# Kernel optimization log

Hardware: AMD Instinct MI355X
Metric: run time of the kernel (lower is better)

Reference implementation:

```python
import jax, jax.numpy as jnp
import numpy as np

NUM_HEADS = 10
LN_EPS = 1e-5


def setup_inputs() -> dict:
    key = jax.random.key(0)
    ks = jax.random.split(key, 6)
    N, D = 4096, 640  # in_dim == out_dim required by residual add
    x = jax.random.normal(ks[0], (N, D), dtype=jnp.float32)
    s = 1.0 / np.sqrt(D)
    Wq = jax.random.normal(ks[1], (D, D), dtype=jnp.float32) * s  # torch Linear weight [out,in]
    Wk = jax.random.normal(ks[2], (D, D), dtype=jnp.float32) * s
    Wv = jax.random.normal(ks[3], (D, D), dtype=jnp.float32) * s
    gamma = jnp.ones((D,), dtype=jnp.float32)
    beta = jnp.zeros((D,), dtype=jnp.float32)
    return {"x": x, "Wq": Wq, "Wk": Wk, "Wv": Wv, "gamma": gamma, "beta": beta}


def reference(x, Wq, Wk, Wv, gamma, beta):
    N, D = x.shape
    dk = D // NUM_HEADS
    Q = x @ Wq.T  # [N, D]
    K = x @ Wk.T
    V = x @ Wv.T
    # Faithful to source: raw reshapes (NOT transposes)
    Qh = Q.reshape(NUM_HEADS, N, dk)
    Kh = K.reshape(NUM_HEADS, N, dk).reshape(NUM_HEADS, dk, N)  # torch.reshape, not .mT
    Vh = V.reshape(NUM_HEADS, N, dk)
    # Faithful quirk: scale by sqrt(K.shape[2]) == sqrt(N)
    scale = np.float32(np.sqrt(N))
    wghts = jax.nn.softmax((Qh @ Kh) / scale, axis=-1)  # [H, N, N]
    values = wghts @ Vh  # [H, N, dk]
    values = values.reshape(N, NUM_HEADS * dk)  # raw reshape merge
    values = values + x  # residual
    # LayerNorm(out_dim), biased variance, eps=1e-5
    mean = jnp.mean(values, axis=-1, keepdims=True)
    var = jnp.mean(jnp.square(values - mean), axis=-1, keepdims=True)
    out = (values - mean) * jax.lax.rsqrt(var + LN_EPS) * gamma + beta
    return out
```

## Files before the change

### kernel.cpp

```cpp
#include <hip/hip_runtime.h>
#if __has_include(<hip/hip_fp8.h>)
#include <hip/hip_fp8.h>
#endif


typedef __bf16 bf16x8 __attribute__((ext_vector_type(8)));
typedef __bf16 bf16x4 __attribute__((ext_vector_type(4)));
typedef float  f32x4  __attribute__((ext_vector_type(4)));
typedef unsigned short u16x4 __attribute__((ext_vector_type(4)));
typedef unsigned int   u32x4 __attribute__((ext_vector_type(4)));
typedef long           la64  __attribute__((may_alias));
typedef unsigned int   ua32  __attribute__((may_alias));

#define N_TOK   4096
#define D_MODEL 640
#define DK      64
#define HSLAB   (N_TOK * DK)
#define SQS 0.15014030f

#if __has_builtin(__builtin_amdgcn_exp2f)
#define EXP2(x) __builtin_amdgcn_exp2f(x)
#else
#define EXP2(x) exp2f(x)
#endif

__device__ __forceinline__ void stage16(const void* g, void* lds_uniform) {
    __builtin_amdgcn_global_load_lds(
        (const __attribute__((address_space(1))) unsigned int*)g,
        (__attribute__((address_space(3))) unsigned int*)lds_uniform, 16, 0, 0);
}

__device__ __forceinline__ u16x4 cvt4(f32x4 v) {
    return __builtin_bit_cast(u16x4, __builtin_convertvector(v, bf16x4));
}

__device__ __forceinline__ unsigned int pk_fp8(f32x4 v) {
#if __has_builtin(__builtin_amdgcn_cvt_pk_fp8_f32)
    int r = 0;
    r = __builtin_amdgcn_cvt_pk_fp8_f32(v[0], v[1], r, false);
    r = __builtin_amdgcn_cvt_pk_fp8_f32(v[2], v[3], r, true);
    return (unsigned int)r;
#else
    union { unsigned char b[4]; unsigned int u; } x;
    x.b[0] = __hip_fp8_e4m3(v[0]).__x;
    x.b[1] = __hip_fp8_e4m3(v[1]).__x;
    x.b[2] = __hip_fp8_e4m3(v[2]).__x;
    x.b[3] = __hip_fp8_e4m3(v[3]).__x;
    return x.u;
#endif
}

__global__ __launch_bounds__(256) void cvt_all(const float* __restrict__ x,
                                               const float* __restrict__ w0,
                                               const float* __restrict__ w1,
                                               const float* __restrict__ w2,
                                               unsigned short* __restrict__ xb,
                                               unsigned short* __restrict__ d0,
                                               unsigned short* __restrict__ d1,
                                               unsigned short* __restrict__ d2,
                                               f32x4* __restrict__ ltot4) {
    int i = blockIdx.x * 256 + threadIdx.x;
    if (i >= 962560) { ltot4[i - 962560] = (f32x4){0.f, 0.f, 0.f, 0.f}; return; }
    const float* s; unsigned short* d; int off; float scl = 1.0f;
    if (i < 655360) { s = x; d = xb; off = i; }
    else {
        int j = i - 655360;
        int w = j / 102400; off = j - w * 102400;
        s = (w == 0) ? w0 : (w == 1) ? w1 : w2;
        d = (w == 0) ? d0 : (w == 1) ? d1 : d2;
        if (w < 2) scl = SQS;
    }
    f32x4 v = ((const f32x4*)s)[off];
    v[0] *= scl; v[1] *= scl; v[2] *= scl; v[3] *= scl;
    ((u16x4*)d)[off] = cvt4(v);
}

__global__ __launch_bounds__(256, 2) void gemm_qkv(
    const unsigned short* __restrict__ xb,
    const unsigned short* __restrict__ wq,
    const unsigned short* __restrict__ wk,
    const unsigned short* __restrict__ wv,
    unsigned short* __restrict__ Qo,
    unsigned short* __restrict__ Ko,
    unsigned short* __restrict__ Vo) {
    const int b = blockIdx.x;
    const int g = b & 31;
    const int r = b >> 5;
    const int mode = r / 5;
    const int m0 = g * 128;
    const int n0 = (r % 5) * 128;
    const unsigned short* W = (mode == 0) ? wq : (mode == 1) ? wk : wv;
    unsigned short*       C = (mode == 0) ? Qo : (mode == 1) ? Ko : Vo;

    __shared__ unsigned short As[8192];
    __shared__ unsigned short Bs[8192];

    const int tid  = threadIdx.x;
    const int lane = tid & 63;
    const int wave = tid >> 6;
    const int quad = lane >> 4, l16 = lane & 15;
    const int wm = (wave >> 1) * 64, wn = (wave & 1) * 64;
    const int swz = l16 & 7;

    f32x4 acc[4][4] = {};

    int prow[4], pcol[4], lbase[4];
    for (int j = 0; j < 4; j++) {
        int p = j * 256 + tid;
        prow[j] = p >> 3;
        pcol[j] = ((p & 7) ^ (prow[j] & 7)) * 8;
        lbase[j] = (j * 256 + wave * 64) * 8;
    }

    for (int kt = 0; kt < D_MODEL; kt += 64) {
        __syncthreads();
        for (int j = 0; j < 4; j++) {
            stage16(&xb[(size_t)(m0 + prow[j]) * D_MODEL + kt + pcol[j]], As + lbase[j]);
            stage16(&W [(size_t)(n0 + prow[j]) * D_MODEL + kt + pcol[j]], Bs + lbase[j]);
        }
        __syncthreads();

        for (int s = 0; s < 2; s++) {
            bf16x8 af[4], bfr[4];
            for (int mi = 0; mi < 4; mi++) {
                int row = wm + mi * 16 + l16;
                af[mi] = *(const bf16x8*)&As[row * 64 + (((s << 2) + quad) ^ swz) * 8];
            }
            for (int ni = 0; ni < 4; ni++) {
                int row = wn + ni * 16 + l16;
                bfr[ni] = *(const bf16x8*)&Bs[row * 64 + (((s << 2) + quad) ^ swz) * 8];
            }
            for (int mi = 0; mi < 4; mi++)
                for (int ni = 0; ni < 4; ni++)
                    acc[mi][ni] = __builtin_amdgcn_mfma_f32_16x16x32_bf16(af[mi], bfr[ni], acc[mi][ni], 0, 0, 0);
        }
    }

    for (int mi = 0; mi < 4; mi++)
        for (int ni = 0; ni < 4; ni++) {
            u16x4 cv = cvt4(acc[mi][ni]);
            for (int r2 = 0; r2 < 4; r2++) {
                int row = m0 + wm + mi * 16 + quad * 4 + r2;
                int col = n0 + wn + ni * 16 + l16;
                C[(size_t)row * D_MODEL + col] = cv[r2];
            }
        }
}

__global__ __launch_bounds__(256) void transpose_kv(
    const unsigned short* __restrict__ Kn, unsigned char* __restrict__ Kp8,
    const unsigned short* __restrict__ Vn, unsigned char* __restrict__ Vp8,
    const unsigned short* __restrict__ Qn, unsigned char* __restrict__ Qf8) {
    const int z = blockIdx.z;
    const int t = threadIdx.x;

    if (z >= 20) {
        const size_t base = (size_t)(z - 20) * HSLAB + blockIdx.x * 4096 + t * 16;
        bf16x8 v0 = *(const bf16x8*)&Qn[base];
        bf16x8 v1 = *(const bf16x8*)&Qn[base + 8];
        f32x4 a = {(float)v0[0], (float)v0[1], (float)v0[2], (float)v0[3]};
        f32x4 b = {(float)v0[4], (float)v0[5], (float)v0[6], (float)v0[7]};
        f32x4 c = {(float)v1[0], (float)v1[1], (float)v1[2], (float)v1[3]};
        f32x4 d = {(float)v1[4], (float)v1[5], (float)v1[6], (float)v1[7]};
        u32x4 o = {pk_fp8(a), pk_fp8(b), pk_fp8(c), pk_fp8(d)};
        *(u32x4*)&Qf8[base] = o;
        return;
    }

    __shared__ unsigned short T[64][66];
    const unsigned short* src; unsigned char* dst;
    int R, Cc, r0, c0;
    if (z < 10) { src = Kn; dst = Kp8; R = 64;   Cc = 4096; r0 = 0; c0 = blockIdx.x * 64; }
    else        { src = Vn; dst = Vp8; R = 4096; Cc = 64;   r0 = blockIdx.x * 64; c0 = 0; }
    const size_t hb = (size_t)(z % 10) * HSLAB;
    const int rr = t >> 3, c8 = (t & 7) * 8;

    for (int hf = 0; hf < 2; hf++) {
        int r = rr + hf * 32;
        bf16x8 v = *(const bf16x8*)&src[hb + (size_t)(r0 + r) * Cc + c0 + c8];
        for (int j = 0; j < 8; j++) T[r][c8 + j] = ((unsigned short*)&v)[j];
    }
    __syncthreads();
    const bf16x8 zz = {};
    for (int hf = 0; hf < 2; hf++) {
        int r = rr + hf * 32;
        *(bf16x8*)&((unsigned short*)src)[hb + (size_t)(r0 + r) * Cc + c0 + c8] = zz;
    }
    for (int hf = 0; hf < 2; hf++) {
        int oc = rr + hf * 32;
        f32x4 lo, hi;
        for (int j = 0; j < 4; j++) {
            lo[j] = __builtin_bit_cast(float, (unsigned int)T[c8 + j][oc] << 16);
            hi[j] = __builtin_bit_cast(float, (unsigned int)T[c8 + 4 + j][oc] << 16);
        }
        uint2 ov; ov.x = pk_fp8(lo); ov.y = pk_fp8(hi);
        size_t dcol = (z < 10) ? ((size_t)(c0 + oc) * 64 + r0 + c8)
                               : ((size_t)oc * 4096 + r0 + c8);
        *(uint2*)&dst[hb + dcol] = ov;
    }
}

__global__ __launch_bounds__(256, 4) void attn(
    const unsigned char* __restrict__ Qf8,
    const unsigned char* __restrict__ Kp8,
    const unsigned char* __restrict__ Vp8,
    float* __restrict__ vals,
    float* __restrict__ l_tot) {
    const int h  = blockIdx.x >> 5;
    const int qt = blockIdx.x & 31;
    const int ntile = (blockIdx.y == 2) ? 10 : 11;
    const int tile0 = blockIdx.y * 11;
    const int lane = threadIdx.x & 63;
    const int wave = threadIdx.x >> 6;
    const int quad = lane >> 4, l16 = lane & 15;
    const size_t hoff = (size_t)h * HSLAB;

    __shared__ unsigned char sm[40960];
    unsigned char* const Kb0 = sm;
    unsigned char* const Kb1 = sm + 8192;
    unsigned char* const Vt  = sm + 16384;
    unsigned char* const Pw  = sm + 24576 + wave * 4096;

    const int qbase = qt * 128 + wave * 32;
    long qd[2][2];
    for (int g = 0; g < 2; g++) {
        const unsigned char* qp = Qf8 + hoff + (size_t)(qbase + g * 16 + l16) * 64 + quad * 8;
        qd[g][0] = *(const la64*)(qp);
        qd[g][1] = *(const la64*)(qp + 32);
    }

    f32x4 o[2][4] = {};
    f32x4 ol[2] = {};
    const long ONES8 = 0x3838383838383838L;

    const int cA = wave * 64 + lane, cB = cA + 256;
    const int kKeyA = ((cA >> 5) << 3) + (cA & 7), kCiA = (cA >> 3) & 3;
    const int kKeyB = ((cB >> 5) << 3) + (cB & 7), kCiB = (cB >> 3) & 3;
    const int vDkA  = ((cA >> 6) << 3) + (cA & 7), vCvA = (cA >> 3) & 7;
    const int vDkB  = ((cB >> 6) << 3) + (cB & 7), vCvB = (cB >> 3) & 7;

    const int kfb = (l16 >> 3) * 512 + (quad >> 1) * 128 + (l16 & 7) * 16 + (quad & 1) * 8;
    const int vfb = (l16 >> 3) * 1024 + (quad >> 1) * 128 + (l16 & 7) * 16 + (quad & 1) * 8;

    {
        const int keyb = tile0 << 7;
        stage16(Kp8 + hoff + (size_t)(keyb + kKeyA) * 64 + kCiA * 16, Kb0 + wave * 1024);
        stage16(Kp8 + hoff + (size_t)(keyb + kKeyB) * 64 + kCiB * 16, Kb0 + 4096 + wave * 1024);
    }

    for (int t = 0; t < ntile; t++) {
        const int keyb = (tile0 + t) << 7;
        unsigned char* const Kcur = (t & 1) ? Kb1 : Kb0;

        __syncthreads();

        if (t + 1 < ntile) {
            const int keyn = (tile0 + t + 1) << 7;
            unsigned char* const Knext = (t & 1) ? Kb0 : Kb1;
            stage16(Kp8 + hoff + (size_t)(keyn + kKeyA) * 64 + kCiA * 16, Knext + wave * 1024);
            stage16(Kp8 + hoff + (size_t)(keyn + kKeyB) * 64 + kCiB * 16, Knext + 4096 + wave * 1024);
        }
        stage16(Vp8 + hoff + (size_t)vDkA * N_TOK + keyb + vCvA * 16, Vt + wave * 1024);
        stage16(Vp8 + hoff + (size_t)vDkB * N_TOK + keyb + vCvB * 16, Vt + 4096 + wave * 1024);

        for (int ni = 0; ni < 8; ni++) {
            const unsigned char* kp = Kcur + ni * 1024 + kfb;
            long a0 = *(const la64*)(kp);
            long a1 = *(const la64*)(kp + 256);
            for (int g = 0; g < 2; g++) {
                f32x4 s = {};
                s = __builtin_amdgcn_mfma_f32_16x16x32_fp8_fp8(a0, qd[g][0], s, 0, 0, 0);
                s = __builtin_amdgcn_mfma_f32_16x16x32_fp8_fp8(a1, qd[g][1], s, 0, 0, 0);
                f32x4 pv;
                for (int r = 0; r < 4; r++) pv[r] = EXP2(s[r]);
                const int pu = ni * 2 + (quad >> 1);
                *(ua32*)(Pw + pu * 256 +
                         (((g * 16 + l16) + ((pu & 3) << 3)) & 31) * 8 +
                         (quad & 1) * 4) = pk_fp8(pv);
            }
        }

        __syncthreads();

        for (int ks = 0; ks < 4; ks++) {
            long vf[4];
            for (int nd = 0; nd < 4; nd++)
                vf[nd] = *(const la64*)(Vt + nd * 2048 + ks * 256 + vfb);
            for (int g = 0; g < 2; g++) {
                long pf = *(const la64*)(Pw + (ks * 4 + quad) * 256 +
                                         (((g * 16 + l16) + (quad << 3)) & 31) * 8);
                ol[g] = __builtin_amdgcn_mfma_f32_16x16x32_fp8_fp8(pf, ONES8, ol[g], 0, 0, 0);
                for (int nd = 0; nd < 4; nd++)
                    o[g][nd] = __builtin_amdgcn_mfma_f32_16x16x32_fp8_fp8(pf, vf[nd], o[g][nd], 0, 0, 0);
            }
        }
    }

    if (l16 == 0)
        for (int g = 0; g < 2; g++)
            for (int r = 0; r < 4; r++)
                atomicAdd(&l_tot[(h << 12) + qbase + g * 16 + quad * 4 + r], ol[g][r]);

    for (int g = 0; g < 2; g++)
        for (int nd = 0; nd < 4; nd++)
            for (int r = 0; r < 4; r++) {
                int q = qbase + g * 16 + quad * 4 + r;
                atomicAdd(&vals[hoff + (size_t)q * DK + nd * 16 + l16], o[g][nd][r]);
            }
}

__global__ __launch_bounds__(256) void ln_kernel(
    const float* __restrict__ vals, const float* __restrict__ l_tot,
    const float* __restrict__ x,
    const float* __restrict__ gamma, const float* __restrict__ beta,
    float* __restrict__ out) {
    const int wave = threadIdx.x >> 6, lane = threadIdx.x & 63;
    const int row  = blockIdx.x * 4 + wave;
    const float* v  = vals + (size_t)row * D_MODEL;
    const float* xr = x    + (size_t)row * D_MODEL;

    float t[10];
    float s = 0.f;
    for (int i = 0; i < 10; i++) {
        float linv = 1.0f / l_tot[row * 10 + i];
        t[i] = v[lane + i * 64] * linv + xr[lane + i * 64];
        s += t[i];
    }
    for (int off = 32; off; off >>= 1) s += __shfl_xor(s, off, 64);
    float mean = s * (1.0f / 640.0f);
    float s2 = 0.f;
    for (int i = 0; i < 10; i++) { float d = t[i] - mean; s2 += d * d; }
    for (int off = 32; off; off >>= 1) s2 += __shfl_xor(s2, off, 64);
    float inv = rsqrtf(s2 * (1.0f / 640.0f) + 1e-5f);

    float* orow = out + (size_t)row * D_MODEL;
    for (int i = 0; i < 10; i++) {
        int c = lane + i * 64;
        orow[c] = (t[i] - mean) * inv * gamma[c] + beta[c];
    }
}

extern "C" void kernel_launch(void* const* d_in, const int* in_sizes, int n_in,
                              void* d_out, int out_size, void* d_ws, size_t ws_size,
                              hipStream_t stream) {
    const float* x     = (const float*)d_in[0];
    const float* Wq    = (const float*)d_in[1];
    const float* Wk    = (const float*)d_in[2];
    const float* Wv    = (const float*)d_in[3];
    const float* gamma = (const float*)d_in[4];
    const float* beta  = (const float*)d_in[5];
    float* out = (float*)d_out;

    char* ws = (char*)d_ws;
    unsigned short* xb  = (unsigned short*)(ws);
    unsigned char*  Qf8 = (unsigned char*)(ws);
    unsigned short* wqb = (unsigned short*)(ws + 5242880);
    unsigned short* wkb = (unsigned short*)(ws + 6062080);
    unsigned short* wvb = (unsigned short*)(ws + 6881280);
    unsigned short* Qn  = (unsigned short*)(ws + 7700480);
    unsigned char*  Kp8 = (unsigned char*)(ws + 12943360);
    unsigned char*  Vp8 = (unsigned char*)(ws + 18186240);
    unsigned short* Kn  = (unsigned short*)(ws + 23429120);
    unsigned short* Vn  = (unsigned short*)(ws + 28672000);
    float*          vals  = (float*)(ws + 23429120);
    float*          l_tot = (float*)(ws + 33914880);

    cvt_all<<<3800, 256, 0, stream>>>(x, Wq, Wk, Wv, xb, wqb, wkb, wvb,
                                      (f32x4*)l_tot);

    gemm_qkv<<<480, 256, 0, stream>>>(xb, wqb, wkb, wvb, Qn, Kn, Vn);

    transpose_kv<<<dim3(64, 1, 30), 256, 0, stream>>>(Kn, Kp8, Vn, Vp8, Qn, Qf8);

    attn<<<dim3(320, 3), 256, 0, stream>>>(Qf8, Kp8, Vp8, vals, l_tot);
    ln_kernel<<<1024, 256, 0, stream>>>(vals, l_tot, x, gamma, beta, out);
}
```

Before: 152.8 us.

## Emit FP8 Q from GEMM, halve attention key tile, add MFMA priority hints

The QKV GEMM now packs the Q output straight to FP8, so the separate Q conversion pass in the transpose kernel goes away. The attention kernel uses 64-key tiles instead of 128 and halves shared memory, and the key range is split four ways with 16 tiles each instead of three ways. This aims to raise occupancy and parallelism, at the cost of more loop iterations, more barriers and more atomics per output. s_setprio hints are wrapped around the MFMA sequences, and the byte-wise FP8 Q stores in the GEMM epilogue are poorly coalesced.

```diff
diff --git a/kernel.cpp b/kernel.cpp
--- a/kernel.cpp
+++ b/kernel.cpp
@@ -80,7 +80,7 @@
     const unsigned short* __restrict__ wq,
     const unsigned short* __restrict__ wk,
     const unsigned short* __restrict__ wv,
-    unsigned short* __restrict__ Qo,
+    unsigned char*  __restrict__ Qf8o,
     unsigned short* __restrict__ Ko,
     unsigned short* __restrict__ Vo) {
     const int b = blockIdx.x;
@@ -90,7 +90,7 @@
     const int m0 = g * 128;
     const int n0 = (r % 5) * 128;
     const unsigned short* W = (mode == 0) ? wq : (mode == 1) ? wk : wv;
-    unsigned short*       C = (mode == 0) ? Qo : (mode == 1) ? Ko : Vo;
+    unsigned short*       C = (mode == 1) ? Ko : Vo;
 
     __shared__ unsigned short As[8192];
     __shared__ unsigned short Bs[8192];
@@ -136,36 +136,34 @@
         }
     }
 
-    for (int mi = 0; mi < 4; mi++)
-        for (int ni = 0; ni < 4; ni++) {
-            u16x4 cv = cvt4(acc[mi][ni]);
-            for (int r2 = 0; r2 < 4; r2++) {
-                int row = m0 + wm + mi * 16 + quad * 4 + r2;
-                int col = n0 + wn + ni * 16 + l16;
-                C[(size_t)row * D_MODEL + col] = cv[r2];
-            }
-        }
+    if (mode == 0) {
+        for (int mi = 0; mi < 4; mi++)
+            for (int ni = 0; ni < 4; ni++) {
+                unsigned int p = pk_fp8(acc[mi][ni]);
+                for (int r2 = 0; r2 < 4; r2++) {
+                    int row = m0 + wm + mi * 16 + quad * 4 + r2;
+                    int col = n0 + wn + ni * 16 + l16;
+                    Qf8o[(size_t)row * D_MODEL + col] = (unsigned char)(p >> (r2 * 8));
+                }
+            }
+    } else {
+        for (int mi = 0; mi < 4; mi++)
+            for (int ni = 0; ni < 4; ni++) {
+                u16x4 cv = cvt4(acc[mi][ni]);
+                for (int r2 = 0; r2 < 4; r2++) {
+                    int row = m0 + wm + mi * 16 + quad * 4 + r2;
+                    int col = n0 + wn + ni * 16 + l16;
+                    C[(size_t)row * D_MODEL + col] = cv[r2];
+                }
+            }
+    }
 }
 
 __global__ __launch_bounds__(256) void transpose_kv(
     const unsigned short* __restrict__ Kn, unsigned char* __restrict__ Kp8,
-    const unsigned short* __restrict__ Vn, unsigned char* __restrict__ Vp8,
-    const unsigned short* __restrict__ Qn, unsigned char* __restrict__ Qf8) {
+    const unsigned short* __restrict__ Vn, unsigned char* __restrict__ Vp8) {
     const int z = blockIdx.z;
     const int t = threadIdx.x;
-
-    if (z >= 20) {
-        const size_t base = (size_t)(z - 20) * HSLAB + blockIdx.x * 4096 + t * 16;
-        bf16x8 v0 = *(const bf16x8*)&Qn[base];
-        bf16x8 v1 = *(const bf16x8*)&Qn[base + 8];
-        f32x4 a = {(float)v0[0], (float)v0[1], (float)v0[2], (float)v0[3]};
-        f32x4 b = {(float)v0[4], (float)v0[5], (float)v0[6], (float)v0[7]};
-        f32x4 c = {(float)v1[0], (float)v1[1], (float)v1[2], (float)v1[3]};
-        f32x4 d = {(float)v1[4], (float)v1[5], (float)v1[6], (float)v1[7]};
-        u32x4 o = {pk_fp8(a), pk_fp8(b), pk_fp8(c), pk_fp8(d)};
-        *(u32x4*)&Qf8[base] = o;
-        return;
-    }
 
     __shared__ unsigned short T[64][66];
     const unsigned short* src; unsigned char* dst;
@@ -208,18 +206,17 @@
     float* __restrict__ l_tot) {
     const int h  = blockIdx.x >> 5;
     const int qt = blockIdx.x & 31;
-    const int ntile = (blockIdx.y == 2) ? 10 : 11;
-    const int tile0 = blockIdx.y * 11;
+    const int tile0 = blockIdx.y * 16;
     const int lane = threadIdx.x & 63;
     const int wave = threadIdx.x >> 6;
     const int quad = lane >> 4, l16 = lane & 15;
     const size_t hoff = (size_t)h * HSLAB;
 
-    __shared__ unsigned char sm[40960];
+    __shared__ unsigned char sm[20480];
     unsigned char* const Kb0 = sm;
-    unsigned char* const Kb1 = sm + 8192;
-    unsigned char* const Vt  = sm + 16384;
-    unsigned char* const Pw  = sm + 24576 + wave * 4096;
+    unsigned char* const Kb1 = sm + 4096;
+    unsigned char* const Vt  = sm + 8192;
+    unsigned char* const Pw  = sm + 12288 + wave * 2048;
 
     const int qbase = qt * 128 + wave * 32;
     long qd[2][2];
@@ -233,44 +230,39 @@
     f32x4 ol[2] = {};
     const long ONES8 = 0x3838383838383838L;
 
-    const int cA = wave * 64 + lane, cB = cA + 256;
-    const int kKeyA = ((cA >> 5) << 3) + (cA & 7), kCiA = (cA >> 3) & 3;
-    const int kKeyB = ((cB >> 5) << 3) + (cB & 7), kCiB = (cB >> 3) & 3;
-    const int vDkA  = ((cA >> 6) << 3) + (cA & 7), vCvA = (cA >> 3) & 7;
-    const int vDkB  = ((cB >> 6) << 3) + (cB & 7), vCvB = (cB >> 3) & 7;
-
-    const int kfb = (l16 >> 3) * 512 + (quad >> 1) * 128 + (l16 & 7) * 16 + (quad & 1) * 8;
-    const int vfb = (l16 >> 3) * 1024 + (quad >> 1) * 128 + (l16 & 7) * 16 + (quad & 1) * 8;
+    const int c = wave * 64 + lane;
+    const int kKey = ((c >> 5) << 3) + (c & 7), kCi = (c >> 3) & 3;
+
+    const int fb = (l16 >> 3) * 512 + (quad >> 1) * 128 + (l16 & 7) * 16 + (quad & 1) * 8;
 
     {
-        const int keyb = tile0 << 7;
-        stage16(Kp8 + hoff + (size_t)(keyb + kKeyA) * 64 + kCiA * 16, Kb0 + wave * 1024);
-        stage16(Kp8 + hoff + (size_t)(keyb + kKeyB) * 64 + kCiB * 16, Kb0 + 4096 + wave * 1024);
-    }
-
-    for (int t = 0; t < ntile; t++) {
-        const int keyb = (tile0 + t) << 7;
+        const int keyb = tile0 << 6;
+        stage16(Kp8 + hoff + (size_t)(keyb + kKey) * 64 + kCi * 16, Kb0 + wave * 1024);
+    }
+
+    for (int t = 0; t < 16; t++) {
+        const int keyb = (tile0 + t) << 6;
         unsigned char* const Kcur = (t & 1) ? Kb1 : Kb0;
 
         __syncthreads();
 
-        if (t + 1 < ntile) {
-            const int keyn = (tile0 + t + 1) << 7;
+        if (t + 1 < 16) {
+            const int keyn = (tile0 + t + 1) << 6;
             unsigned char* const Knext = (t & 1) ? Kb0 : Kb1;
-            stage16(Kp8 + hoff + (size_t)(keyn + kKeyA) * 64 + kCiA * 16, Knext + wave * 1024);
-            stage16(Kp8 + hoff + (size_t)(keyn + kKeyB) * 64 + kCiB * 16, Knext + 4096 + wave * 1024);
-        }
-        stage16(Vp8 + hoff + (size_t)vDkA * N_TOK + keyb + vCvA * 16, Vt + wave * 1024);
-        stage16(Vp8 + hoff + (size_t)vDkB * N_TOK + keyb + vCvB * 16, Vt + 4096 + wave * 1024);
-
-        for (int ni = 0; ni < 8; ni++) {
-            const unsigned char* kp = Kcur + ni * 1024 + kfb;
+            stage16(Kp8 + hoff + (size_t)(keyn + kKey) * 64 + kCi * 16, Knext + wave * 1024);
+        }
+        stage16(Vp8 + hoff + (size_t)kKey * N_TOK + keyb + kCi * 16, Vt + wave * 1024);
+
+        for (int ni = 0; ni < 4; ni++) {
+            const unsigned char* kp = Kcur + ni * 1024 + fb;
             long a0 = *(const la64*)(kp);
             long a1 = *(const la64*)(kp + 256);
             for (int g = 0; g < 2; g++) {
                 f32x4 s = {};
+                __builtin_amdgcn_s_setprio(1);
                 s = __builtin_amdgcn_mfma_f32_16x16x32_fp8_fp8(a0, qd[g][0], s, 0, 0, 0);
                 s = __builtin_amdgcn_mfma_f32_16x16x32_fp8_fp8(a1, qd[g][1], s, 0, 0, 0);
+                __builtin_amdgcn_s_setprio(0);
                 f32x4 pv;
                 for (int r = 0; r < 4; r++) pv[r] = EXP2(s[r]);
                 const int pu = ni * 2 + (quad >> 1);
@@ -282,16 +274,18 @@
 
         __syncthreads();
 
-        for (int ks = 0; ks < 4; ks++) {
+        for (int ks = 0; ks < 2; ks++) {
             long vf[4];
             for (int nd = 0; nd < 4; nd++)
-                vf[nd] = *(const la64*)(Vt + nd * 2048 + ks * 256 + vfb);
+                vf[nd] = *(const la64*)(Vt + nd * 1024 + ks * 256 + fb);
             for (int g = 0; g < 2; g++) {
                 long pf = *(const la64*)(Pw + (ks * 4 + quad) * 256 +
                                          (((g * 16 + l16) + (quad << 3)) & 31) * 8);
+                __builtin_amdgcn_s_setprio(1);
                 ol[g] = __builtin_amdgcn_mfma_f32_16x16x32_fp8_fp8(pf, ONES8, ol[g], 0, 0, 0);
                 for (int nd = 0; nd < 4; nd++)
                     o[g][nd] = __builtin_amdgcn_mfma_f32_16x16x32_fp8_fp8(pf, vf[nd], o[g][nd], 0, 0, 0);
+                __builtin_amdgcn_s_setprio(0);
             }
         }
     }
@@ -353,11 +347,10 @@
 
     char* ws = (char*)d_ws;
     unsigned short* xb  = (unsigned short*)(ws);
-    unsigned char*  Qf8 = (unsigned char*)(ws);
     unsigned short* wqb = (unsigned short*)(ws + 5242880);
     unsigned short* wkb = (unsigned short*)(ws + 6062080);
     unsigned short* wvb = (unsigned short*)(ws + 6881280);
-    unsigned short* Qn  = (unsigned short*)(ws + 7700480);
+    unsigned char*  Qf8 = (unsigned char*)(ws + 7700480);
     unsigned char*  Kp8 = (unsigned char*)(ws + 12943360);
     unsigned char*  Vp8 = (unsigned char*)(ws + 18186240);
     unsigned short* Kn  = (unsigned short*)(ws + 23429120);
@@ -368,10 +361,10 @@
     cvt_all<<<3800, 256, 0, stream>>>(x, Wq, Wk, Wv, xb, wqb, wkb, wvb,
                                       (f32x4*)l_tot);
 
-    gemm_qkv<<<480, 256, 0, stream>>>(xb, wqb, wkb, wvb, Qn, Kn, Vn);
-
-    transpose_kv<<<dim3(64, 1, 30), 256, 0, stream>>>(Kn, Kp8, Vn, Vp8, Qn, Qf8);
-
-    attn<<<dim3(320, 3), 256, 0, stream>>>(Qf8, Kp8, Vp8, vals, l_tot);
+    gemm_qkv<<<480, 256, 0, stream>>>(xb, wqb, wkb, wvb, Qf8, Kn, Vn);
+
+    transpose_kv<<<dim3(64, 1, 20), 256, 0, stream>>>(Kn, Kp8, Vn, Vp8);
+
+    attn<<<dim3(320, 4), 256, 0, stream>>>(Qf8, Kp8, Vp8, vals, l_tot);
     ln_kernel<<<1024, 256, 0, stream>>>(vals, l_tot, x, gamma, beta, out);
 }
```

New measurement: 157.6 us. +3.1%, slower.
